# Performance work log

Measured on AMD Instinct MI355X. Metric: run time of the kernel, lower is better.

## Reference

```python
import jax, jax.numpy as jnp
import numpy as np
import math

TOP_K = 2
CAP_FACTOR = 1.25
AUX_W = 0.01


def setup_inputs() -> dict:
    key = jax.random.key(0)
    k1, k2 = jax.random.split(key)
    x = jax.random.normal(k1, (8192, 4096), dtype=jnp.float32)
    # gate weight, torch init std=0.01, stored as (E, D) like nn.Linear
    gate_w = jax.random.normal(k2, (64, 4096), dtype=jnp.float32) * 0.01
    return {"x": x, "gate_w": gate_w}


def reference(x, gate_w):
    N, D = x.shape
    E = gate_w.shape[0]
    K = TOP_K
    C = max(math.ceil(CAP_FACTOR * N / E), 1)  # expert capacity

    logits = x @ gate_w.T                      # (N, E)
    probs = jax.nn.softmax(logits, axis=-1)    # (N, E)
    vals, idx = jax.lax.top_k(probs, K)        # (N, K)
    vals = vals / vals.sum(axis=-1, keepdims=True)

    # Parallel replacement of the serial double loop: flatten (N,K) row-major
    # (token-major, then k) which matches the loop iteration order exactly.
    flat_e = idx.reshape(-1)                               # (N*K,) expert ids
    oh = jax.nn.one_hot(flat_e, E, dtype=jnp.int32)        # (N*K, E)
    # exclusive prefix count of prior assignments to each expert
    pos = jnp.cumsum(oh, axis=0) - oh                      # (N*K, E)
    slot = jnp.take_along_axis(pos, flat_e[:, None], axis=1)[:, 0]  # (N*K,)
    # In the torch loop the counter saturates at C (only incremented when
    # c < C), so slot==prior_total is equivalent: kept iff prior_total < C.
    keep = slot < C
    slot_s = jnp.where(keep, slot, 0)
    tok = jnp.arange(N * K) // K

    combine_weights = jnp.zeros((N, E, C), dtype=x.dtype).at[
        tok, flat_e, slot_s].add(jnp.where(keep, vals.reshape(-1), 0.0))
    dispatch_mask = (jnp.zeros((N, E, C), dtype=jnp.int32).at[
        tok, flat_e, slot_s].add(keep.astype(jnp.int32))) > 0

    # load balancing loss
    f = oh.astype(jnp.float32).reshape(N, K, E).mean(axis=(0, 1))  # (E,)
    p = probs.mean(axis=0)                                         # (E,)
    load_loss = AUX_W * E * jnp.sum(f * p)

    return dispatch_mask, combine_weights, probs, load_loss
```

## Files before the change

### kernel.cpp

```cpp
#include <hip/hip_runtime.h>
#include <math.h>

#define N_TOK 8192
#define DIM   4096
#define NEXP  64
#define CAP   160
#define OFF_CW    (83886080ULL)
#define OFF_PROBS (167772160ULL)
#define OFF_LOSS  (168296448ULL)
#define NA    16384

typedef float vfloat4 __attribute__((ext_vector_type(4)));

__device__ __forceinline__ float wave_max64(float v) {
    for (int m = 1; m < 64; m <<= 1) v = fmaxf(v, __shfl_xor(v, m, 64));
    return v;
}
__device__ __forceinline__ float wave_sum64(float v) {
    for (int m = 1; m < 64; m <<= 1) v += __shfl_xor(v, m, 64);
    return v;
}
__device__ __forceinline__ void wave_argmax64(float& v, int& i) {
    for (int m = 1; m < 64; m <<= 1) {
        float ov = __shfl_xor(v, m, 64);
        int   oi = __shfl_xor(i, m, 64);
        if (ov > v || (ov == v && oi < i)) { v = ov; i = oi; }
    }
}

__global__ __launch_bounds__(256) void k_gemm(const float* __restrict__ x,
                                              const float* __restrict__ gw,
                                              float* __restrict__ part, int dps) {
    __shared__ float xs[64][68];
    __shared__ float wsh[64][68];
    const int tb = blockIdx.x * 64;
    const int d_begin = blockIdx.y * dps;
    const int t  = threadIdx.x;
    const int tx = t & 15, ty = t >> 4;
    float acc[4][4] = {};
    for (int ci = 0; ci < dps / 64; ++ci) {
        const int d0 = d_begin + ci * 64;
        for (int it = 0; it < 4; ++it) {
            int idx = t + 256 * it;
            int row = idx >> 4;
            int d4  = idx & 15;
            *(float4*)(&xs[row][4 * d4]) =
                *(const float4*)(x + (size_t)(tb + row) * DIM + d0 + 4 * d4);
            *(float4*)(&wsh[row][4 * d4]) =
                *(const float4*)(gw + (size_t)row * DIM + d0 + 4 * d4);
        }
        __syncthreads();
        for (int d4 = 0; d4 < 16; ++d4) {
            float4 xa[4], wb[4];
            for (int i = 0; i < 4; ++i) xa[i] = *(const float4*)(&xs[ty + 16 * i][4 * d4]);
            for (int j = 0; j < 4; ++j) wb[j] = *(const float4*)(&wsh[tx + 16 * j][4 * d4]);
            for (int i = 0; i < 4; ++i)
                for (int j = 0; j < 4; ++j) {
                    acc[i][j] = fmaf(xa[i].x, wb[j].x, acc[i][j]);
                    acc[i][j] = fmaf(xa[i].y, wb[j].y, acc[i][j]);
                    acc[i][j] = fmaf(xa[i].z, wb[j].z, acc[i][j]);
                    acc[i][j] = fmaf(xa[i].w, wb[j].w, acc[i][j]);
                }
        }
        __syncthreads();
    }
    for (int i = 0; i < 4; ++i)
        for (int j = 0; j < 4; ++j)
            part[(size_t)blockIdx.y * N_TOK * NEXP +
                 (size_t)(tb + ty + 16 * i) * NEXP + (tx + 16 * j)] = acc[i][j];
}

__global__ __launch_bounds__(256) void k_router(const float* __restrict__ part, int S,
                                                float* __restrict__ probs_out,
                                                int* __restrict__ rec_e,
                                                float* __restrict__ rec_w) {
    const int tok  = blockIdx.x * 4 + (threadIdx.x >> 6);
    const int lane = threadIdx.x & 63;
    float l = 0.f;
    for (int s = 0; s < S; ++s)
        l += part[(size_t)s * N_TOK * NEXP + (size_t)tok * NEXP + lane];
    const float m  = wave_max64(l);
    const float ex = expf(l - m);
    const float sm = wave_sum64(ex);
    const float p  = ex / sm;
    probs_out[(size_t)tok * NEXP + lane] = p;
    float v1 = p; int i1 = lane;
    wave_argmax64(v1, i1);
    float v2 = (lane == i1) ? -1.f : p; int i2 = lane;
    wave_argmax64(v2, i2);
    if (lane == 0) {
        const float denom = v1 + v2;
        rec_e[2 * tok]     = i1;
        rec_e[2 * tok + 1] = i2;
        rec_w[2 * tok]     = v1 / denom;
        rec_w[2 * tok + 1] = v2 / denom;
    }
}

__global__ __launch_bounds__(256) void k_preduce(const float* __restrict__ probs,
                                                 float* __restrict__ psum_part) {
    __shared__ float sh[256];
    const int e = threadIdx.x & 63, tg = threadIdx.x >> 6;
    const int tok0 = blockIdx.x * 128;
    float a = 0.f;
    for (int k = 0; k < 32; ++k)
        a += probs[(size_t)(tok0 + tg + 4 * k) * NEXP + e];
    sh[threadIdx.x] = a;
    __syncthreads();
    if (threadIdx.x < 64)
        psum_part[blockIdx.x * 64 + threadIdx.x] =
            sh[threadIdx.x] + sh[64 + threadIdx.x] +
            sh[128 + threadIdx.x] + sh[192 + threadIdx.x];
}

__global__ __launch_bounds__(256) void k_assign(const int* __restrict__ rec_e,
                                                int* __restrict__ rec_s,
                                                int* __restrict__ ecnt) {
    const int w    = blockIdx.x * 4 + (threadIdx.x >> 6);
    const int lane = threadIdx.x & 63;
    int base = 0;
    const unsigned long long ltmask = (1ull << lane) - 1ull;
    for (int c = 0; c < NA / 64; ++c) {
        const int i = c * 64 + lane;
        const int e = rec_e[i];
        const unsigned long long mask = __ballot(e == w);
        if (e == w) {
            const int slot = base + __popcll(mask & ltmask);
            rec_s[i] = (slot < CAP) ? slot : -1;
        }
        base += __popcll(mask);
    }
    if (lane == 0) ecnt[w] = base;
}

__global__ __launch_bounds__(256) void k_write(const int* __restrict__ rec_e,
                                               const int* __restrict__ rec_s,
                                               const float* __restrict__ rec_w,
                                               const int* __restrict__ ecnt,
                                               const float* __restrict__ psum_part,
                                               float* __restrict__ out) {
    const int tok = blockIdx.x;
    if (tok == N_TOK) {
        if (threadIdx.x < 64) {
            const int e = threadIdx.x;
            float ps = 0.f;
            for (int b = 0; b < 64; ++b) ps += psum_part[b * 64 + e];
            float term = ((float)ecnt[e] / (float)NA) * (ps / (float)N_TOK);
            term = wave_sum64(term);
            if (e == 0) out[OFF_LOSS] = 0.01f * 64.f * term;
        }
        return;
    }
    const int e1 = rec_e[2 * tok], e2 = rec_e[2 * tok + 1];
    const int s1 = rec_s[2 * tok], s2 = rec_s[2 * tok + 1];
    const float w1 = rec_w[2 * tok], w2 = rec_w[2 * tok + 1];
    const int p1 = (s1 >= 0) ? e1 * CAP + s1 : -1;
    const int p2 = (s2 >= 0) ? e2 * CAP + s2 : -1;
    const int o1 = (p1 >= 0) ? (p1 >> 2) : -1, c1 = p1 & 3;
    const int o2 = (p2 >= 0) ? (p2 >> 2) : -1, c2 = p2 & 3;
    float* dm = out + (size_t)tok * (NEXP * CAP);
    float* cw = out + OFF_CW + (size_t)tok * (NEXP * CAP);
    for (int it = 0; it < 10; ++it) {
        const int o = it * 256 + threadIdx.x;
        vfloat4 d = {0.f, 0.f, 0.f, 0.f};
        vfloat4 c = {0.f, 0.f, 0.f, 0.f};
        if (o == o1) { d[c1] = 1.f; c[c1] = w1; }
        if (o == o2) { d[c2] = 1.f; c[c2] = w2; }
        __builtin_nontemporal_store(d, (vfloat4*)(dm + 4 * o));
        __builtin_nontemporal_store(c, (vfloat4*)(cw + 4 * o));
    }
}

extern "C" void kernel_launch(void* const* d_in, const int* in_sizes, int n_in,
                              void* d_out, int out_size, void* d_ws, size_t ws_size,
                              hipStream_t stream) {
    const float* x  = (const float*)d_in[0];
    const float* gw = (const float*)d_in[1];
    float* out = (float*)d_out;

    int S = 8;
    const size_t fixed = (size_t)(3 * NA + 64 * 64 + 64) * 4;
    while (S > 1 && ws_size < (size_t)S * N_TOK * NEXP * 4 + fixed) S >>= 1;

    char* w = (char*)d_ws;
    float* part      = (float*)w;
    int*   rec_e     = (int*)(w + (size_t)S * N_TOK * NEXP * 4);
    float* rec_w     = (float*)((char*)rec_e + NA * 4);
    int*   rec_s     = (int*)((char*)rec_w + NA * 4);
    float* psum_part = (float*)((char*)rec_s + NA * 4);
    int*   ecnt      = (int*)((char*)psum_part + 64 * 64 * 4);

    dim3 g1(128, S);
    k_gemm<<<g1, 256, 0, stream>>>(x, gw, part, DIM / S);
    k_router<<<2048, 256, 0, stream>>>(part, S, out + OFF_PROBS, rec_e, rec_w);
    k_preduce<<<64, 256, 0, stream>>>(out + OFF_PROBS, psum_part);
    k_assign<<<16, 256, 0, stream>>>(rec_e, rec_s, ecnt);
    k_write<<<N_TOK + 1, 256, 0, stream>>>(rec_e, rec_s, rec_w, ecnt, psum_part, out);
}
```

Before: 864.1 us.

## Overlap output zeroing with gate GEMM and replace dense write with sparse scatter

Zero-filling of the large dispatch_mask and combine_weights buffers is moved into extra blocks of the GEMM launch, so the write-bound fill can overlap the compute-bound matmul. The final per-token dense write kernel becomes a small scatter that writes only the kept assignments. It also fixes the split count at 8 instead of sizing it from the workspace, which assumes the workspace is large enough. The scatter relies on the zero-fill having finished earlier in stream order.

```diff
diff --git a/kernel.cpp b/kernel.cpp
--- a/kernel.cpp
+++ b/kernel.cpp
@@ -9,6 +9,7 @@
 #define OFF_PROBS (167772160ULL)
 #define OFF_LOSS  (168296448ULL)
 #define NA    16384
+#define SPLIT 8
 
 typedef float vfloat4 __attribute__((ext_vector_type(4)));
 
@@ -28,17 +29,31 @@
     }
 }
 
-__global__ __launch_bounds__(256) void k_gemm(const float* __restrict__ x,
-                                              const float* __restrict__ gw,
-                                              float* __restrict__ part, int dps) {
+__global__ __launch_bounds__(256) void k_zero_gemm(const float* __restrict__ x,
+                                                   const float* __restrict__ gw,
+                                                   float* __restrict__ part,
+                                                   float* __restrict__ out) {
+    if (blockIdx.x >= 1024) {
+        const int tok = blockIdx.x - 1024;
+        float* dm = out + (size_t)tok * (NEXP * CAP);
+        float* cw = out + OFF_CW + (size_t)tok * (NEXP * CAP);
+        const vfloat4 z = {0.f, 0.f, 0.f, 0.f};
+        for (int it = 0; it < 10; ++it) {
+            const int o = 4 * (it * 256 + threadIdx.x);
+            __builtin_nontemporal_store(z, (vfloat4*)(dm + o));
+            __builtin_nontemporal_store(z, (vfloat4*)(cw + o));
+        }
+        return;
+    }
     __shared__ float xs[64][68];
     __shared__ float wsh[64][68];
-    const int tb = blockIdx.x * 64;
-    const int d_begin = blockIdx.y * dps;
+    const int tb = (blockIdx.x & 127) * 64;
+    const int sy = blockIdx.x >> 7;
+    const int d_begin = sy * (DIM / SPLIT);
     const int t  = threadIdx.x;
     const int tx = t & 15, ty = t >> 4;
     float acc[4][4] = {};
-    for (int ci = 0; ci < dps / 64; ++ci) {
+    for (int ci = 0; ci < (DIM / SPLIT) / 64; ++ci) {
         const int d0 = d_begin + ci * 64;
         for (int it = 0; it < 4; ++it) {
             int idx = t + 256 * it;
@@ -66,18 +81,18 @@
     }
     for (int i = 0; i < 4; ++i)
         for (int j = 0; j < 4; ++j)
-            part[(size_t)blockIdx.y * N_TOK * NEXP +
+            part[(size_t)sy * N_TOK * NEXP +
                  (size_t)(tb + ty + 16 * i) * NEXP + (tx + 16 * j)] = acc[i][j];
 }
 
-__global__ __launch_bounds__(256) void k_router(const float* __restrict__ part, int S,
+__global__ __launch_bounds__(256) void k_router(const float* __restrict__ part,
                                                 float* __restrict__ probs_out,
                                                 int* __restrict__ rec_e,
                                                 float* __restrict__ rec_w) {
     const int tok  = blockIdx.x * 4 + (threadIdx.x >> 6);
     const int lane = threadIdx.x & 63;
     float l = 0.f;
-    for (int s = 0; s < S; ++s)
+    for (int s = 0; s < SPLIT; ++s)
         l += part[(size_t)s * N_TOK * NEXP + (size_t)tok * NEXP + lane];
     const float m  = wave_max64(l);
     const float ex = expf(l - m);
@@ -133,14 +148,13 @@
     if (lane == 0) ecnt[w] = base;
 }
 
-__global__ __launch_bounds__(256) void k_write(const int* __restrict__ rec_e,
-                                               const int* __restrict__ rec_s,
-                                               const float* __restrict__ rec_w,
-                                               const int* __restrict__ ecnt,
-                                               const float* __restrict__ psum_part,
-                                               float* __restrict__ out) {
-    const int tok = blockIdx.x;
-    if (tok == N_TOK) {
+__global__ __launch_bounds__(256) void k_scatter(const int* __restrict__ rec_e,
+                                                 const int* __restrict__ rec_s,
+                                                 const float* __restrict__ rec_w,
+                                                 const int* __restrict__ ecnt,
+                                                 const float* __restrict__ psum_part,
+                                                 float* __restrict__ out) {
+    if (blockIdx.x == 64) {
         if (threadIdx.x < 64) {
             const int e = threadIdx.x;
             float ps = 0.f;
@@ -151,23 +165,14 @@
         }
         return;
     }
-    const int e1 = rec_e[2 * tok], e2 = rec_e[2 * tok + 1];
-    const int s1 = rec_s[2 * tok], s2 = rec_s[2 * tok + 1];
-    const float w1 = rec_w[2 * tok], w2 = rec_w[2 * tok + 1];
-    const int p1 = (s1 >= 0) ? e1 * CAP + s1 : -1;
-    const int p2 = (s2 >= 0) ? e2 * CAP + s2 : -1;
-    const int o1 = (p1 >= 0) ? (p1 >> 2) : -1, c1 = p1 & 3;
-    const int o2 = (p2 >= 0) ? (p2 >> 2) : -1, c2 = p2 & 3;
-    float* dm = out + (size_t)tok * (NEXP * CAP);
-    float* cw = out + OFF_CW + (size_t)tok * (NEXP * CAP);
-    for (int it = 0; it < 10; ++it) {
-        const int o = it * 256 + threadIdx.x;
-        vfloat4 d = {0.f, 0.f, 0.f, 0.f};
-        vfloat4 c = {0.f, 0.f, 0.f, 0.f};
-        if (o == o1) { d[c1] = 1.f; c[c1] = w1; }
-        if (o == o2) { d[c2] = 1.f; c[c2] = w2; }
-        __builtin_nontemporal_store(d, (vfloat4*)(dm + 4 * o));
-        __builtin_nontemporal_store(c, (vfloat4*)(cw + 4 * o));
+    const int i = blockIdx.x * 256 + threadIdx.x;
+    const int s = rec_s[i];
+    if (s >= 0) {
+        const int tok = i >> 1;
+        const int e   = rec_e[i];
+        const size_t off = (size_t)tok * (NEXP * CAP) + (size_t)e * CAP + s;
+        out[off]          = 1.0f;
+        out[OFF_CW + off] = rec_w[i];
     }
 }
 
@@ -178,22 +183,17 @@
     const float* gw = (const float*)d_in[1];
     float* out = (float*)d_out;
 
-    int S = 8;
-    const size_t fixed = (size_t)(3 * NA + 64 * 64 + 64) * 4;
-    while (S > 1 && ws_size < (size_t)S * N_TOK * NEXP * 4 + fixed) S >>= 1;
-
     char* w = (char*)d_ws;
     float* part      = (float*)w;
-    int*   rec_e     = (int*)(w + (size_t)S * N_TOK * NEXP * 4);
+    int*   rec_e     = (int*)(w + (size_t)SPLIT * N_TOK * NEXP * 4);
     float* rec_w     = (float*)((char*)rec_e + NA * 4);
     int*   rec_s     = (int*)((char*)rec_w + NA * 4);
     float* psum_part = (float*)((char*)rec_s + NA * 4);
     int*   ecnt      = (int*)((char*)psum_part + 64 * 64 * 4);
 
-    dim3 g1(128, S);
-    k_gemm<<<g1, 256, 0, stream>>>(x, gw, part, DIM / S);
-    k_router<<<2048, 256, 0, stream>>>(part, S, out + OFF_PROBS, rec_e, rec_w);
+    k_zero_gemm<<<1024 + N_TOK, 256, 0, stream>>>(x, gw, part, out);
+    k_router<<<2048, 256, 0, stream>>>(part, out + OFF_PROBS, rec_e, rec_w);
     k_preduce<<<64, 256, 0, stream>>>(out + OFF_PROBS, psum_part);
     k_assign<<<16, 256, 0, stream>>>(rec_e, rec_s, ecnt);
-    k_write<<<N_TOK + 1, 256, 0, stream>>>(rec_e, rec_s, rec_w, ecnt, psum_part, out);
+    k_scatter<<<65, 256, 0, stream>>>(rec_e, rec_s, rec_w, ecnt, psum_part, out);
 }
```

Result: no change. 854.6 us (-1.1%).
